# Kernel optimization log

Hardware: AMD Instinct MI355X
Metric: run time of the kernel (lower is better)

The kernel has to match this reference:

```python
import jax, jax.numpy as jnp
import numpy as np

B, CIN, COUT, HIN = 2, 64, 64, 96
ALPHA = 0.2       # LeakyReLU slope in GAT
K_RANK = 6        # dist.argsort(1).argsort(1) <= 6  -> 7 nearest neighbors incl. self
DN = ('NCHW', 'OIHW', 'NCHW')


def setup_inputs():
    key = jax.random.key(0)
    ks = jax.random.split(key, 10)
    sc = lambda k, shape, s: jax.random.normal(k, shape, jnp.float32) * s
    return {
        'x': jax.random.normal(ks[0], (B, CIN, HIN, HIN), jnp.float32),
        'conv_w': sc(ks[1], (COUT, CIN, 3, 3), 0.05),
        'conv_b': jnp.zeros((COUT,), jnp.float32),
        'W1': sc(ks[2], (COUT, COUT), 0.1),
        'a1': sc(ks[3], (2 * COUT,), 0.1),
        'W2': sc(ks[4], (COUT, COUT), 0.1),
        'a2': sc(ks[5], (2 * COUT,), 0.1),
        'Wout': sc(ks[6], (2 * COUT, COUT), 0.1),
        'aout': sc(ks[7], (2 * COUT,), 0.1),
        'tconv_w': sc(ks[8], (COUT, COUT, 3, 3), 0.05),  # torch ConvTranspose2d layout [in,out,kh,kw]
        'tconv_b': jnp.zeros((COUT,), jnp.float32),
    }


def _gat_layer(h, adj, W, a, concat):
    # h: [B,N,F_in], W: [F_in,F_out], a: [2*F_out]
    Wh = h @ W                                   # [B,N,F']
    Fo = W.shape[1]
    e = (Wh @ a[:Fo])[:, :, None] + (Wh @ a[Fo:])[:, None, :]   # [B,N,N]
    e = jax.nn.leaky_relu(e, ALPHA)
    e = jnp.where(adj > 0, e, -9e15)
    attn = jax.nn.softmax(e, axis=-1)
    out = jnp.einsum('bij,bjf->bif', attn, Wh)
    return jax.nn.elu(out) if concat else out


def reference(x, conv_w, conv_b, W1, a1, W2, a2, Wout, aout, tconv_w, tconv_b):
    # --- Pre_ProcessLayer_Graph: stride-2 conv, flatten, 7-NN dense adjacency ---
    y = jax.lax.conv_general_dilated(x, conv_w, (2, 2), ((1, 1), (1, 1)),
                                     dimension_numbers=DN) + conv_b[None, :, None, None]
    Bb, C, H, W_ = y.shape
    N = H * W_
    feat = y.reshape(Bb, C, N).transpose(0, 2, 1)          # [B,N,C]
    sq = jnp.sum(feat * feat, axis=-1)                     # [B,N]
    d2 = sq[:, :, None] + sq[:, None, :] - 2.0 * jnp.einsum('bic,bjc->bij', feat, feat)
    dist = jnp.sqrt(jnp.maximum(d2, 0.0))                  # euclidean cdist
    ranks = jnp.argsort(jnp.argsort(dist, axis=-1), axis=-1)
    adj = (ranks <= K_RANK).astype(feat.dtype)             # [B,N,N] binary, incl. self (rank 0)
    # --- GAT (pyGAT style): 2 concat heads + output attention layer, eval mode ---
    h1 = _gat_layer(feat, adj, W1, a1, True)
    h2 = _gat_layer(feat, adj, W2, a2, True)
    hcat = jnp.concatenate([h1, h2], axis=-1)              # [B,N,2C]
    g = jax.nn.elu(_gat_layer(hcat, adj, Wout, aout, False))  # [B,N,C]
    # --- reshape back + transpose conv (k=3, s=2, p=1, output_padding=1) ---
    g = g.transpose(0, 2, 1).reshape(Bb, C, H, W_)
    wt = jnp.flip(tconv_w, (2, 3)).transpose(1, 0, 2, 3)   # -> [out,in,kh,kw]
    out = jax.lax.conv_general_dilated(g, wt, (1, 1), ((1, 2), (1, 2)),
                                       lhs_dilation=(2, 2),
                                       dimension_numbers=DN) + tconv_b[None, :, None, None]
    return out
```

## Files before the change

kernel.cpp:

```cpp
#include <hip/hip_runtime.h>
#include <hip/hip_bf16.h>
#include <stdint.h>

using bf16 = __hip_bfloat16;
using u64 = unsigned long long;

constexpr int B_ = 2;
constexpr int N_ = 2304;

constexpr int OFF_WC2   = 0;
constexpr int OFF_WT2   = 36864;
constexpr int OFF_W1F   = 73728;
constexpr int OFF_W2F   = 77824;
constexpr int OFF_WOUTF = 81920;
constexpr int OFF_A1F   = 90112;
constexpr int OFF_A2F   = 90240;
constexpr int OFF_AOUTF = 90368;
constexpr int OFF_CBF   = 90496;
constexpr int OFF_TBF   = 90560;
constexpr int OFF_FLAG  = 90624;
constexpr int OFF_SQ    = 90688;
constexpr int OFF_S11   = 95296;
constexpr int OFF_S12   = 99904;
constexpr int OFF_S21   = 104512;
constexpr int OFF_S22   = 109120;
constexpr int OFF_S1O   = 113728;
constexpr int OFF_S2O   = 118336;
constexpr int OFF_KNN   = 122944;
constexpr int OFF_BUF0  = 159808;
constexpr int OFF_BUF1  = 454720;
constexpr int OFF_BUF2  = 749632;
constexpr int OFF_BUF3  = 1044544;
constexpr int OFF_PK    = 1339456;

__device__ __forceinline__ float bf2f_raw(unsigned short u) {
    return __uint_as_float(((unsigned int)u) << 16);
}

__device__ __forceinline__ unsigned int mono32(float f) {
    unsigned int u = __float_as_uint(f);
    return (u & 0x80000000u) ? ~u : (u | 0x80000000u);
}

__device__ __forceinline__ bool detect_f32(const void* conv_w) {
    const unsigned short* cw = (const unsigned short*)conv_w;
    float m = 0.f;
    #pragma unroll
    for (int u = 0; u < 64; ++u) {
        float v = fabsf(bf2f_raw(cw[u]));
        if (v < 3.0e38f) m = fmaxf(m, v);
    }
    return m > 1.0e4f;
}

__global__ __launch_bounds__(256) void kc_prep(
    const void* conv_w, const void* conv_b, const void* W1, const void* a1,
    const void* W2, const void* a2, const void* Wout, const void* aout,
    const void* tconv_w, const void* tconv_b, float* __restrict__ ws)
{
    bool f32 = detect_f32(conv_w);
    int idx = blockIdx.x * 256 + threadIdx.x;
    if (idx == 0) ws[OFF_FLAG] = f32 ? 1.f : 0.f;
    if (idx < 32256) ws[OFF_SQ + idx] = 0.f;

    {
        int tap = idx >> 12, ic = (idx >> 6) & 63, oc = idx & 63;
        if (f32) {
            ws[OFF_WC2 + idx] = ((const float*)conv_w)[(oc * 64 + ic) * 9 + tap];
            ws[OFF_WT2 + idx] = ((const float*)tconv_w)[(ic * 64 + oc) * 9 + tap];
        } else {
            ws[OFF_WC2 + idx] = bf2f_raw(((const unsigned short*)conv_w)[(oc * 64 + ic) * 9 + tap]);
            ws[OFF_WT2 + idx] = bf2f_raw(((const unsigned short*)tconv_w)[(ic * 64 + oc) * 9 + tap]);
        }
    }
    if (idx < 4096) {
        if (f32) {
            ws[OFF_W1F + idx] = ((const float*)W1)[idx];
            ws[OFF_W2F + idx] = ((const float*)W2)[idx];
        } else {
            ws[OFF_W1F + idx] = bf2f_raw(((const unsigned short*)W1)[idx]);
            ws[OFF_W2F + idx] = bf2f_raw(((const unsigned short*)W2)[idx]);
        }
    }
    if (idx < 8192)
        ws[OFF_WOUTF + idx] = f32 ? ((const float*)Wout)[idx]
                                  : bf2f_raw(((const unsigned short*)Wout)[idx]);
    if (idx < 128) {
        if (f32) {
            ws[OFF_A1F + idx]   = ((const float*)a1)[idx];
            ws[OFF_A2F + idx]   = ((const float*)a2)[idx];
            ws[OFF_AOUTF + idx] = ((const float*)aout)[idx];
        } else {
            ws[OFF_A1F + idx]   = bf2f_raw(((const unsigned short*)a1)[idx]);
            ws[OFF_A2F + idx]   = bf2f_raw(((const unsigned short*)a2)[idx]);
            ws[OFF_AOUTF + idx] = bf2f_raw(((const unsigned short*)aout)[idx]);
        }
    }
    if (idx < 64) {
        if (f32) {
            ws[OFF_CBF + idx] = ((const float*)conv_b)[idx];
            ws[OFF_TBF + idx] = ((const float*)tconv_b)[idx];
        } else {
            ws[OFF_CBF + idx] = bf2f_raw(((const unsigned short*)conv_b)[idx]);
            ws[OFF_TBF + idx] = bf2f_raw(((const unsigned short*)tconv_b)[idx]);
        }
    }
}

template <bool F32>
__device__ __forceinline__ void conv_body(const void* __restrict__ x,
                                          float* __restrict__ ws,
                                          int n, int ocb, int b)
{
    int oy = n / 48, ox = n - (n / 48) * 48;
    const float* wc2 = ws + OFF_WC2;
    size_t xb = (size_t)b * 64 * 9216;
    float acc[4] = {0, 0, 0, 0};

    for (int ky = 0; ky < 3; ++ky) {
        int iy = 2 * oy - 1 + ky;
        bool vy = (unsigned)iy < 96u;
        int iyc = vy ? iy : 0;
        for (int kx = 0; kx < 3; ++kx) {
            int ix = 2 * ox - 1 + kx;
            bool v = vy && ((unsigned)ix < 96u);
            int ixc = v ? ix : 0;
            size_t xoff = xb + iyc * 96 + ixc;
            const float* wb = wc2 + (ky * 3 + kx) * 4096 + ocb;
            #pragma unroll 8
            for (int ic = 0; ic < 64; ++ic) {
                float xv;
                if (F32) xv = ((const float*)x)[xoff + ic * 9216];
                else     xv = bf2f_raw(((const unsigned short*)x)[xoff + ic * 9216]);
                xv = v ? xv : 0.f;
                const float* wr = wb + ic * 64;
                #pragma unroll
                for (int o = 0; o < 4; ++o) acc[o] += xv * wr[o];
            }
        }
    }
    float* featT = ws + OFF_BUF0 + (size_t)b * 64 * N_;
    const float* cb = ws + OFF_CBF;
    float ssum = 0.f;
    #pragma unroll
    for (int o = 0; o < 4; ++o) {
        float f = acc[o] + cb[ocb + o];
        acc[o] = f;
        featT[(ocb + o) * N_ + n] = f;
        ssum += f * f;
    }
    *(float4*)(ws + OFF_BUF2 + ((size_t)(b * N_ + n) * 64 + ocb)) =
        make_float4(acc[0], acc[1], acc[2], acc[3]);
    atomicAdd(ws + OFF_SQ + b * N_ + n, ssum);
}

__global__ __launch_bounds__(128) void k1_conv(const void* __restrict__ x,
                                               float* __restrict__ ws)
{
    int n   = blockIdx.x * 128 + threadIdx.x;
    int ocb = blockIdx.y * 4;
    int b   = blockIdx.z;
    if (ws[OFF_FLAG] != 0.f) conv_body<true >(x, ws, n, ocb, b);
    else                     conv_body<false>(x, ws, n, ocb, b);
}

__global__ __launch_bounds__(256) void k2_knn(float* __restrict__ ws)
{
    __shared__ float As[16][64];
    __shared__ float Bs[64][128];
    int tid = threadIdx.x;
    int i0  = blockIdx.x * 16;
    int jh  = blockIdx.y;
    int b   = i0 / N_;
    const float* fT = ws + OFF_BUF0 + (size_t)b * 64 * N_;
    const float* sq = ws + OFF_SQ + b * N_;
    int w = tid >> 6, lane = tid & 63;
    int r0 = w * 4;

    {
        int r = tid >> 4, c4 = tid & 15;
        float4 v = ((const float4*)(ws + OFF_BUF2))[(size_t)(i0 + r) * 16 + c4];
        *(float4*)&As[r][c4 * 4] = v;
    }

    u64 K[4][7];
    #pragma unroll
    for (int r = 0; r < 4; ++r)
        #pragma unroll
        for (int t = 0; t < 7; ++t) K[r][t] = ~0ull;

    __syncthreads();

    for (int jt = 0; jt < 6; ++jt) {
        int jb = jh * 768 + jt * 128;
        #pragma unroll
        for (int it = 0; it < 8; ++it) {
            int idx = tid + it * 256;
            int k = idx >> 5, j4 = idx & 31;
            float4 v = *(const float4*)(fT + (size_t)k * N_ + jb + j4 * 4);
            *(float4*)&Bs[k][j4 * 4] = v;
        }
        __syncthreads();

        int jA = jb + 2 * lane, jB = jA + 1;
        float accA[4] = {0, 0, 0, 0};
        float accB[4] = {0, 0, 0, 0};
        #pragma unroll 4
        for (int k4 = 0; k4 < 16; ++k4) {
            float4 av[4];
            #pragma unroll
            for (int r = 0; r < 4; ++r)
                av[r] = *(const float4*)&As[r0 + r][k4 * 4];
            float2 p0 = *(const float2*)&Bs[k4 * 4 + 0][2 * lane];
            float2 p1 = *(const float2*)&Bs[k4 * 4 + 1][2 * lane];
            float2 p2 = *(const float2*)&Bs[k4 * 4 + 2][2 * lane];
            float2 p3 = *(const float2*)&Bs[k4 * 4 + 3][2 * lane];
            #pragma unroll
            for (int r = 0; r < 4; ++r) {
                accA[r] += av[r].x * p0.x + av[r].y * p1.x + av[r].z * p2.x + av[r].w * p3.x;
                accB[r] += av[r].x * p0.y + av[r].y * p1.y + av[r].z * p2.y + av[r].w * p3.y;
            }
        }

        float sqA = sq[jA], sqB = sq[jB];
        #pragma unroll
        for (int r = 0; r < 4; ++r) {
            #pragma unroll
            for (int q = 0; q < 2; ++q) {
                int j = q ? jB : jA;
                float y = (q ? sqB : sqA) - 2.f * (q ? accB[r] : accA[r]);
                u64 key = ((u64)mono32(y) << 32) | (unsigned int)j;
                if (key < K[r][6]) {
                    int pos = 0;
                    #pragma unroll
                    for (int s = 0; s < 7; ++s) pos += (K[r][s] < key) ? 1 : 0;
                    #pragma unroll
                    for (int p = 6; p > 0; --p)
                        K[r][p] = (p == pos) ? key : ((p > pos) ? K[r][p - 1] : K[r][p]);
                    if (pos == 0) K[r][0] = key;
                }
            }
        }
        __syncthreads();
    }

    u64* pk = (u64*)(ws + OFF_PK);
    #pragma unroll
    for (int r = 0; r < 4; ++r) {
        u64 myk = 0;
        for (int pass = 0; pass < 7; ++pass) {
            u64 m = K[r][0];
            #pragma unroll
            for (int s = 1; s < 7; ++s) m = (K[r][s] < m) ? K[r][s] : m;
            #pragma unroll
            for (int off = 1; off < 64; off <<= 1) {
                u64 o = (u64)__shfl_xor((long long)m, off);
                m = (o < m) ? o : m;
            }
            #pragma unroll
            for (int s = 0; s < 7; ++s)
                if (K[r][s] == m) K[r][s] = ~0ull;
            if (lane == pass) myk = m;
        }
        if (lane < 7)
            pk[((size_t)(i0 + r0 + r) * 3 + jh) * 8 + lane] = myk;
    }
}

__global__ __launch_bounds__(256) void k_lin(float* __restrict__ ws)
{
    int g = blockIdx.y;
    if (g == 32) {
        int row = blockIdx.x * 256 + threadIdx.x;
        const u64* pk = (const u64*)(ws + OFF_PK) + (size_t)row * 24;
        int* kout = (int*)(ws + OFF_KNN) + (size_t)row * 8;
        u64 L0[7], L1[7], L2[7];
        #pragma unroll
        for (int q = 0; q < 7; ++q) { L0[q] = pk[q]; L1[q] = pk[8 + q]; L2[q] = pk[16 + q]; }
        #pragma unroll
        for (int q = 0; q < 7; ++q) {
            int rank = q;
            #pragma unroll
            for (int p = 0; p < 7; ++p)
                rank += ((L1[p] < L0[q]) ? 1 : 0) + ((L2[p] < L0[q]) ? 1 : 0);
            if (rank < 7) kout[rank] = (int)(L0[q] & 0xffffffffull);
        }
        #pragma unroll
        for (int q = 0; q < 7; ++q) {
            int rank = q;
            #pragma unroll
            for (int p = 0; p < 7; ++p)
                rank += ((L0[p] < L1[q]) ? 1 : 0) + ((L2[p] < L1[q]) ? 1 : 0);
            if (rank < 7) kout[rank] = (int)(L1[q] & 0xffffffffull);
        }
        #pragma unroll
        for (int q = 0; q < 7; ++q) {
            int rank = q;
            #pragma unroll
            for (int p = 0; p < 7; ++p)
                rank += ((L0[p] < L2[q]) ? 1 : 0) + ((L1[p] < L2[q]) ? 1 : 0);
            if (rank < 7) kout[rank] = (int)(L2[q] & 0xffffffffull);
        }
        return;
    }
    int layer = g >> 4;
    int ocb = (g & 15) * 4;
    const float* W  = ws + (layer ? OFF_W2F : OFF_W1F);
    const float* a  = ws + (layer ? OFF_A2F : OFF_A1F);
    float* out_nc   = ws + (layer ? OFF_BUF3 : OFF_BUF1);
    float* s1       = ws + (layer ? OFF_S21 : OFF_S11);
    float* s2       = ws + (layer ? OFF_S22 : OFF_S12);
    int i = blockIdx.x * 256 + threadIdx.x;
    int b = i / N_, n = i - b * N_;
    const float* in_b = ws + OFF_BUF0 + (size_t)b * 64 * N_;

    float acc[4] = {0, 0, 0, 0};
    #pragma unroll 8
    for (int kk = 0; kk < 64; ++kk) {
        float xv = in_b[kk * N_ + n];
        const float* wr = W + kk * 64 + ocb;
        #pragma unroll
        for (int o = 0; o < 4; ++o) acc[o] += xv * wr[o];
    }
    *(float4*)(out_nc + ((size_t)i * 64 + ocb)) =
        make_float4(acc[0], acc[1], acc[2], acc[3]);
    float p1 = 0.f, p2 = 0.f;
    #pragma unroll
    for (int o = 0; o < 4; ++o) {
        p1 += acc[o] * a[ocb + o];
        p2 += acc[o] * a[64 + ocb + o];
    }
    atomicAdd(s1 + i, p1);
    atomicAdd(s2 + i, p2);
}

__global__ __launch_bounds__(256) void k_lin2(float* __restrict__ ws)
{
    int ocb = blockIdx.y * 4;
    int i = blockIdx.x * 256 + threadIdx.x;
    int b = i / N_, n = i - b * N_;
    const float* h1 = ws + OFF_BUF2 + (size_t)b * 64 * N_;
    const float* h2 = ws + OFF_BUF0 + (size_t)b * 64 * N_;
    const float* W  = ws + OFF_WOUTF;
    const float* a  = ws + OFF_AOUTF;

    float acc[4] = {0, 0, 0, 0};
    #pragma unroll 8
    for (int kk = 0; kk < 64; ++kk) {
        float xv = h1[kk * N_ + n];
        const float* wr = W + kk * 64 + ocb;
        #pragma unroll
        for (int o = 0; o < 4; ++o) acc[o] += xv * wr[o];
    }
    #pragma unroll 8
    for (int kk = 0; kk < 64; ++kk) {
        float xv = h2[kk * N_ + n];
        const float* wr = W + (64 + kk) * 64 + ocb;
        #pragma unroll
        for (int o = 0; o < 4; ++o) acc[o] += xv * wr[o];
    }
    *(float4*)(ws + OFF_BUF1 + ((size_t)i * 64 + ocb)) =
        make_float4(acc[0], acc[1], acc[2], acc[3]);
    float p1 = 0.f, p2 = 0.f;
    #pragma unroll
    for (int o = 0; o < 4; ++o) {
        p1 += acc[o] * a[ocb + o];
        p2 += acc[o] * a[64 + ocb + o];
    }
    atomicAdd(ws + OFF_S1O + i, p1);
    atomicAdd(ws + OFF_S2O + i, p2);
}

__device__ __forceinline__ void attn_body(
    const float* __restrict__ Wh_nc, const float* __restrict__ s1,
    const float* __restrict__ s2, const int* __restrict__ knn,
    float* __restrict__ out, int i, int b, int n, int c4)
{
    const int* kp = knn + (size_t)i * 8;
    int j[7];
    #pragma unroll
    for (int t = 0; t < 7; ++t) {
        int jt = kp[t];
        j[t] = ((unsigned)jt < (unsigned)N_) ? jt : 0;
    }
    float si = s1[i];
    const float* s2b = s2 + b * N_;
    float e[7];
    #pragma unroll
    for (int t = 0; t < 7; ++t) {
        float v = si + s2b[j[t]];
        e[t] = v > 0.f ? v : 0.2f * v;
    }
    float m = e[0];
    #pragma unroll
    for (int t = 1; t < 7; ++t) m = fmaxf(m, e[t]);
    float ssum = 0.f;
    #pragma unroll
    for (int t = 0; t < 7; ++t) { e[t] = __expf(e[t] - m); ssum += e[t]; }
    float inv = 1.f / ssum;
    #pragma unroll
    for (int t = 0; t < 7; ++t) e[t] *= inv;

    const float4* W4 = (const float4*)Wh_nc;
    float4 acc = make_float4(0.f, 0.f, 0.f, 0.f);
    #pragma unroll
    for (int t = 0; t < 7; ++t) {
        float4 v = W4[(size_t)(b * N_ + j[t]) * 16 + c4];
        acc.x += e[t] * v.x; acc.y += e[t] * v.y;
        acc.z += e[t] * v.z; acc.w += e[t] * v.w;
    }
    acc.x = acc.x > 0.f ? acc.x : expm1f(acc.x);
    acc.y = acc.y > 0.f ? acc.y : expm1f(acc.y);
    acc.z = acc.z > 0.f ? acc.z : expm1f(acc.z);
    acc.w = acc.w > 0.f ? acc.w : expm1f(acc.w);
    float* ob = out + (size_t)b * 64 * N_;
    ob[(c4 * 4 + 0) * N_ + n] = acc.x;
    ob[(c4 * 4 + 1) * N_ + n] = acc.y;
    ob[(c4 * 4 + 2) * N_ + n] = acc.z;
    ob[(c4 * 4 + 3) * N_ + n] = acc.w;
}

__global__ __launch_bounds__(256) void k_attn12(float* __restrict__ ws)
{
    int layer = blockIdx.z;
    const float* Wh_nc = ws + (layer ? OFF_BUF3 : OFF_BUF1);
    const float* s1    = ws + (layer ? OFF_S21 : OFF_S11);
    const float* s2    = ws + (layer ? OFF_S22 : OFF_S12);
    float* out         = ws + (layer ? OFF_BUF0 : OFF_BUF2);
    int c4 = blockIdx.y;
    int i = blockIdx.x * 256 + threadIdx.x;
    int b = i / N_, n = i - b * N_;
    attn_body(Wh_nc, s1, s2, (const int*)(ws + OFF_KNN), out, i, b, n, c4);
}

__global__ __launch_bounds__(256) void k_attn_out(float* __restrict__ ws)
{
    int c4 = blockIdx.y;
    int i = blockIdx.x * 256 + threadIdx.x;
    int b = i / N_, n = i - b * N_;
    attn_body(ws + OFF_BUF1, ws + OFF_S1O, ws + OFF_S2O,
              (const int*)(ws + OFF_KNN), ws + OFF_BUF3, i, b, n, c4);
}

__global__ __launch_bounds__(128) void k7_tconv(float* __restrict__ ws,
                                                void* __restrict__ outp)
{
    bool f32 = ws[OFF_FLAG] != 0.f;
    int pixc = blockIdx.x * 128 + threadIdx.x;
    int g    = blockIdx.y;
    int pc   = g >> 3, ocb = (g & 7) * 8;
    int b    = blockIdx.z;
    int py = pc >> 1, px = pc & 1;
    int ay = pixc / 48, bx = pixc - (pixc / 48) * 48;
    int oy = 2 * ay + py, ox = 2 * bx + px;

    const float* gT  = ws + OFF_BUF3 + (size_t)b * 64 * N_;
    const float* wt2 = ws + OFF_WT2;
    float acc[8] = {0, 0, 0, 0, 0, 0, 0, 0};

    int nky = py ? 2 : 1;
    int nkx = px ? 2 : 1;
    for (int s = 0; s < nky; ++s) {
        int ky = py ? (s == 0 ? 0 : 2) : 1;
        int iy = py ? (s == 0 ? ay + 1 : ay) : ay;
        bool vy = iy < 48;
        for (int t = 0; t < nkx; ++t) {
            int kx = px ? (t == 0 ? 0 : 2) : 1;
            int ix = px ? (t == 0 ? bx + 1 : bx) : bx;
            bool v = vy && (ix < 48);
            const float* gp = gT + (v ? iy * 48 + ix : 0);
            const float* wb = wt2 + (ky * 3 + kx) * 4096 + ocb;
            #pragma unroll 8
            for (int ic = 0; ic < 64; ++ic) {
                float gv = gp[ic * N_];
                gv = v ? gv : 0.f;
                const float* wr = wb + ic * 64;
                #pragma unroll
                for (int o = 0; o < 8; ++o) acc[o] += gv * wr[o];
            }
        }
    }
    const float* tb = ws + OFF_TBF;
    size_t base = ((size_t)(b * 64 + ocb) * 96 + oy) * 96 + ox;
    if (f32) {
        float* op = (float*)outp;
        #pragma unroll
        for (int o = 0; o < 8; ++o) op[base + (size_t)o * 9216] = acc[o] + tb[ocb + o];
    } else {
        bf16* op = (bf16*)outp;
        #pragma unroll
        for (int o = 0; o < 8; ++o)
            op[base + (size_t)o * 9216] = __float2bfloat16(acc[o] + tb[ocb + o]);
    }
}

extern "C" void kernel_launch(void* const* d_in, const int* in_sizes, int n_in,
                              void* d_out, int out_size, void* d_ws, size_t ws_size,
                              hipStream_t stream)
{
    float* ws = (float*)d_ws;

    hipLaunchKernelGGL(kc_prep, dim3(144), dim3(256), 0, stream,
                       d_in[1], d_in[2], d_in[3], d_in[4], d_in[5], d_in[6],
                       d_in[7], d_in[8], d_in[9], d_in[10], ws);
    hipLaunchKernelGGL(k1_conv, dim3(18, 16, 2), dim3(128), 0, stream, d_in[0], ws);
    hipLaunchKernelGGL(k2_knn, dim3(288, 3), dim3(256), 0, stream, ws);
    hipLaunchKernelGGL(k_lin, dim3(18, 33), dim3(256), 0, stream, ws);
    hipLaunchKernelGGL(k_attn12, dim3(18, 16, 2), dim3(256), 0, stream, ws);
    hipLaunchKernelGGL(k_lin2, dim3(18, 16), dim3(256), 0, stream, ws);
    hipLaunchKernelGGL(k_attn_out, dim3(18, 16), dim3(256), 0, stream, ws);
    hipLaunchKernelGGL(k7_tconv, dim3(18, 32, 2), dim3(128), 0, stream, ws, d_out);
}
```

Baseline: 247.5 us.

## Restructure kNN kernel: larger row tile, staged distances, per-row 8-lane top-k

Each k2_knn block now handles 32 query rows and 256-column tiles. A rows are read through scalar (wave-uniform) loads instead of shared memory, and each thread computes an 8x4 tile of distances. The distances are staged in shared memory so that 8 lanes share the top-7 selection for one row, rather than every lane holding four 7-entry lists. The final merge then needs only a 3-step shuffle, which cuts register pressure, insertion work and divergence, at the cost of an extra LDS round-trip and more barriers.

```diff
diff --git a/kernel.cpp b/kernel.cpp
--- a/kernel.cpp
+++ b/kernel.cpp
@@ -166,104 +166,110 @@
 
 __global__ __launch_bounds__(256) void k2_knn(float* __restrict__ ws)
 {
-    __shared__ float As[16][64];
-    __shared__ float Bs[64][128];
+    __shared__ float Bs[32][256];
+    __shared__ float ys[32][260];
     int tid = threadIdx.x;
-    int i0  = blockIdx.x * 16;
+    int i0  = blockIdx.x * 32;
     int jh  = blockIdx.y;
     int b   = i0 / N_;
-    const float* fT = ws + OFF_BUF0 + (size_t)b * 64 * N_;
-    const float* sq = ws + OFF_SQ + b * N_;
+    const float* fT  = ws + OFF_BUF0 + (size_t)b * 64 * N_;
+    const float* fnc = ws + OFF_BUF2;
+    const float* sq  = ws + OFF_SQ + b * N_;
     int w = tid >> 6, lane = tid & 63;
-    int r0 = w * 4;
-
-    {
-        int r = tid >> 4, c4 = tid & 15;
-        float4 v = ((const float4*)(ws + OFF_BUF2))[(size_t)(i0 + r) * 16 + c4];
-        *(float4*)&As[r][c4 * 4] = v;
-    }
-
-    u64 K[4][7];
-    #pragma unroll
-    for (int r = 0; r < 4; ++r)
-        #pragma unroll
-        for (int t = 0; t < 7; ++t) K[r][t] = ~0ull;
-
-    __syncthreads();
-
-    for (int jt = 0; jt < 6; ++jt) {
-        int jb = jh * 768 + jt * 128;
-        #pragma unroll
-        for (int it = 0; it < 8; ++it) {
-            int idx = tid + it * 256;
-            int k = idx >> 5, j4 = idx & 31;
-            float4 v = *(const float4*)(fT + (size_t)k * N_ + jb + j4 * 4);
-            *(float4*)&Bs[k][j4 * 4] = v;
-        }
-        __syncthreads();
-
-        int jA = jb + 2 * lane, jB = jA + 1;
-        float accA[4] = {0, 0, 0, 0};
-        float accB[4] = {0, 0, 0, 0};
-        #pragma unroll 4
-        for (int k4 = 0; k4 < 16; ++k4) {
-            float4 av[4];
+    int r0 = w * 8;
+    int arow0 = __builtin_amdgcn_readfirstlane(i0 + r0);
+
+    u64 K[7];
+    #pragma unroll
+    for (int t = 0; t < 7; ++t) K[t] = ~0ull;
+
+    int rsel = r0 + (lane >> 3);
+    int g    = lane & 7;
+
+    for (int jt = 0; jt < 3; ++jt) {
+        int jb = jh * 768 + jt * 256;
+        float acc[8][4];
+        #pragma unroll
+        for (int r = 0; r < 8; ++r)
             #pragma unroll
-            for (int r = 0; r < 4; ++r)
-                av[r] = *(const float4*)&As[r0 + r][k4 * 4];
-            float2 p0 = *(const float2*)&Bs[k4 * 4 + 0][2 * lane];
-            float2 p1 = *(const float2*)&Bs[k4 * 4 + 1][2 * lane];
-            float2 p2 = *(const float2*)&Bs[k4 * 4 + 2][2 * lane];
-            float2 p3 = *(const float2*)&Bs[k4 * 4 + 3][2 * lane];
+            for (int c = 0; c < 4; ++c) acc[r][c] = 0.f;
+
+        for (int kh = 0; kh < 2; ++kh) {
+            __syncthreads();
             #pragma unroll
-            for (int r = 0; r < 4; ++r) {
-                accA[r] += av[r].x * p0.x + av[r].y * p1.x + av[r].z * p2.x + av[r].w * p3.x;
-                accB[r] += av[r].x * p0.y + av[r].y * p1.y + av[r].z * p2.y + av[r].w * p3.y;
+            for (int it = 0; it < 8; ++it) {
+                int idx = tid + it * 256;
+                int k = idx >> 6, j4 = idx & 63;
+                float4 v = *(const float4*)(fT + (size_t)(kh * 32 + k) * N_ + jb + j4 * 4);
+                *(float4*)&Bs[k][j4 * 4] = v;
             }
-        }
-
-        float sqA = sq[jA], sqB = sq[jB];
-        #pragma unroll
-        for (int r = 0; r < 4; ++r) {
-            #pragma unroll
-            for (int q = 0; q < 2; ++q) {
-                int j = q ? jB : jA;
-                float y = (q ? sqB : sqA) - 2.f * (q ? accB[r] : accA[r]);
-                u64 key = ((u64)mono32(y) << 32) | (unsigned int)j;
-                if (key < K[r][6]) {
-                    int pos = 0;
-                    #pragma unroll
-                    for (int s = 0; s < 7; ++s) pos += (K[r][s] < key) ? 1 : 0;
-                    #pragma unroll
-                    for (int p = 6; p > 0; --p)
-                        K[r][p] = (p == pos) ? key : ((p > pos) ? K[r][p - 1] : K[r][p]);
-                    if (pos == 0) K[r][0] = key;
+            __syncthreads();
+
+            #pragma unroll 2
+            for (int k4 = 0; k4 < 8; ++k4) {
+                float4 Bv[4];
+                #pragma unroll
+                for (int kk = 0; kk < 4; ++kk)
+                    Bv[kk] = *(const float4*)&Bs[k4 * 4 + kk][4 * lane];
+                #pragma unroll
+                for (int r = 0; r < 8; ++r) {
+                    float4 a = *(const float4*)(fnc + (size_t)(arow0 + r) * 64
+                                                + kh * 32 + k4 * 4);
+                    acc[r][0] += a.x * Bv[0].x + a.y * Bv[1].x + a.z * Bv[2].x + a.w * Bv[3].x;
+                    acc[r][1] += a.x * Bv[0].y + a.y * Bv[1].y + a.z * Bv[2].y + a.w * Bv[3].y;
+                    acc[r][2] += a.x * Bv[0].z + a.y * Bv[1].z + a.z * Bv[2].z + a.w * Bv[3].z;
+                    acc[r][3] += a.x * Bv[0].w + a.y * Bv[1].w + a.z * Bv[2].w + a.w * Bv[3].w;
                 }
             }
         }
+
+        float4 sqv = *(const float4*)(sq + jb + 4 * lane);
+        #pragma unroll
+        for (int r = 0; r < 8; ++r) {
+            float4 yv;
+            yv.x = sqv.x - 2.f * acc[r][0];
+            yv.y = sqv.y - 2.f * acc[r][1];
+            yv.z = sqv.z - 2.f * acc[r][2];
+            yv.w = sqv.w - 2.f * acc[r][3];
+            *(float4*)&ys[r0 + r][4 * lane] = yv;
+        }
+
+        #pragma unroll 8
+        for (int u = 0; u < 32; ++u) {
+            int jl = g + 8 * u;
+            float y = ys[rsel][jl];
+            u64 key = ((u64)mono32(y) << 32) | (unsigned int)(jb + jl);
+            if (key < K[6]) {
+                int pos = 0;
+                #pragma unroll
+                for (int s = 0; s < 7; ++s) pos += (K[s] < key) ? 1 : 0;
+                #pragma unroll
+                for (int p = 6; p > 0; --p)
+                    K[p] = (p == pos) ? key : ((p > pos) ? K[p - 1] : K[p]);
+                if (pos == 0) K[0] = key;
+            }
+        }
         __syncthreads();
     }
 
-    u64* pk = (u64*)(ws + OFF_PK);
-    #pragma unroll
-    for (int r = 0; r < 4; ++r) {
-        u64 myk = 0;
-        for (int pass = 0; pass < 7; ++pass) {
-            u64 m = K[r][0];
-            #pragma unroll
-            for (int s = 1; s < 7; ++s) m = (K[r][s] < m) ? K[r][s] : m;
-            #pragma unroll
-            for (int off = 1; off < 64; off <<= 1) {
-                u64 o = (u64)__shfl_xor((long long)m, off);
-                m = (o < m) ? o : m;
-            }
-            #pragma unroll
-            for (int s = 0; s < 7; ++s)
-                if (K[r][s] == m) K[r][s] = ~0ull;
-            if (lane == pass) myk = m;
-        }
-        if (lane < 7)
-            pk[((size_t)(i0 + r0 + r) * 3 + jh) * 8 + lane] = myk;
+    u64 myk = 0;
+    for (int pass = 0; pass < 7; ++pass) {
+        u64 m = K[0];
+        #pragma unroll
+        for (int s = 1; s < 7; ++s) m = (K[s] < m) ? K[s] : m;
+        #pragma unroll
+        for (int off = 1; off < 8; off <<= 1) {
+            u64 o = (u64)__shfl_xor((long long)m, off);
+            m = (o < m) ? o : m;
+        }
+        #pragma unroll
+        for (int s = 0; s < 7; ++s)
+            if (K[s] == m) K[s] = ~0ull;
+        if (g == pass) myk = m;
+    }
+    if (g < 7) {
+        u64* pk = (u64*)(ws + OFF_PK);
+        pk[((size_t)(i0 + rsel) * 3 + jh) * 8 + g] = myk;
     }
 }
 
@@ -504,7 +510,7 @@
                        d_in[1], d_in[2], d_in[3], d_in[4], d_in[5], d_in[6],
                        d_in[7], d_in[8], d_in[9], d_in[10], ws);
     hipLaunchKernelGGL(k1_conv, dim3(18, 16, 2), dim3(128), 0, stream, d_in[0], ws);
-    hipLaunchKernelGGL(k2_knn, dim3(288, 3), dim3(256), 0, stream, ws);
+    hipLaunchKernelGGL(k2_knn, dim3(144, 3), dim3(256), 0, stream, ws);
     hipLaunchKernelGGL(k_lin, dim3(18, 33), dim3(256), 0, stream, ws);
     hipLaunchKernelGGL(k_attn12, dim3(18, 16, 2), dim3(256), 0, stream, ws);
     hipLaunchKernelGGL(k_lin2, dim3(18, 16), dim3(256), 0, stream, ws);
```

Result: faster. 238.1 us (-3.8%).
